# Optimization experiments

Hardware: AMD Instinct MI355X
Metric: run time of the kernel (lower is better)

Reference implementation:

```python
import jax, jax.numpy as jnp
import numpy as np

N_HEAD = 16
N_KV_HEAD = 4
HEAD_DIM = 128
RMS_EPS = 1.1920928955078125e-07  # torch float32 eps used by F.rms_norm default


def apply_rotary_emb(x, cos, sin):
    # x: [B,T,H,D]; cos/sin: [1,T,1,D/2]
    d = x.shape[-1] // 2
    x1, x2 = x[..., :d], x[..., d:]
    return jnp.concatenate([x1 * cos + x2 * sin, -x1 * sin + x2 * cos], axis=-1)


def rms_norm(x):
    return x * jax.lax.rsqrt(jnp.mean(x * x, axis=-1, keepdims=True) + RMS_EPS)


def setup_inputs() -> dict:
    key = jax.random.key(0)
    ks = jax.random.split(key, 7)
    B, T, C = 2, 2048, 2048
    return {
        "x": jax.random.normal(ks[0], (B, T, C), jnp.float32),
        "cos": jax.random.normal(ks[1], (1, T, 1, HEAD_DIM // 2), jnp.float32),
        "sin": jax.random.normal(ks[2], (1, T, 1, HEAD_DIM // 2), jnp.float32),
        "wq": jax.random.normal(ks[3], (C, N_HEAD * HEAD_DIM), jnp.float32) * 0.02,
        "wk": jax.random.normal(ks[4], (C, N_KV_HEAD * HEAD_DIM), jnp.float32) * 0.02,
        "wv": jax.random.normal(ks[5], (C, N_KV_HEAD * HEAD_DIM), jnp.float32) * 0.02,
        "wo": jax.random.normal(ks[6], (C, C), jnp.float32) * 0.02,
        "window_size": 512,
    }


def reference(x, cos, sin, wq, wk, wv, wo, window_size):
    B, T, C = x.shape
    H, KV, D = N_HEAD, N_KV_HEAD, HEAD_DIM
    rep = H // KV
    q = (x @ wq).reshape(B, T, H, D)
    k = (x @ wk).reshape(B, T, KV, D)
    v = (x @ wv).reshape(B, T, KV, D)
    q = rms_norm(apply_rotary_emb(q, cos, sin))
    k = rms_norm(apply_rotary_emb(k, cos, sin))
    # GQA: group query heads by kv head instead of materializing expanded K/V
    qg = q.reshape(B, T, KV, rep, D)
    scale = 1.0 / np.sqrt(D)
    scores = jnp.einsum('btkrd,bskd->bkrts', qg, k) * scale  # [B,KV,rep,T,S]
    row = jnp.arange(T)[:, None]
    col = jnp.arange(T)[None, :]
    mask = (col <= row) & (row - col <= window_size)  # causal & sliding window
    scores = jnp.where(mask, scores, jnp.finfo(scores.dtype).min)
    probs = jax.nn.softmax(scores, axis=-1)
    y = jnp.einsum('bkrts,bskd->btkrd', probs, v).reshape(B, T, H * D)
    return y @ wo
```

## Files before the change

kernel.cpp:

```cpp
#include <hip/hip_runtime.h>
#include <stdint.h>

typedef __attribute__((ext_vector_type(4))) float f32x4;
typedef __attribute__((ext_vector_type(8))) __bf16 bf16x8;
typedef __attribute__((ext_vector_type(4))) unsigned int u32x4;
typedef unsigned short u16;

#define B_DIM 2
#define T_DIM 2048
#define C_DIM 2048
#define H_Q   16
#define H_KV  4
#define HD    128
#define NQKV  3072
#define MTOK  4096
#define RMS_EPS 1.1920928955078125e-07f
#define Q_SCALE 0.12751749f

__device__ __forceinline__ u16 f2bf(float f) {
  union { float f; unsigned int u; } v; v.f = f;
  unsigned int r = v.u + 0x7FFFu + ((v.u >> 16) & 1u);
  return (u16)(r >> 16);
}
__device__ __forceinline__ float bf2f(u16 h) {
  union { unsigned int u; float f; } v; v.u = ((unsigned int)h) << 16;
  return v.f;
}
__device__ __forceinline__ f32x4 mfma16(bf16x8 a, bf16x8 b, f32x4 c) {
  return __builtin_amdgcn_mfma_f32_16x16x32_bf16(a, b, c, 0, 0, 0);
}
__device__ __forceinline__ void gl_lds16(const void* g, void* l) {
  __builtin_amdgcn_global_load_lds(
      (const __attribute__((address_space(1))) unsigned int*)g,
      (__attribute__((address_space(3))) unsigned int*)l, 16, 0, 0);
}

__global__ __launch_bounds__(256) void prep_kernel(const float* __restrict__ x,
                                                   const float* __restrict__ wq,
                                                   const float* __restrict__ wk,
                                                   const float* __restrict__ wv,
                                                   const float* __restrict__ wo,
                                                   u16* __restrict__ xb,
                                                   u16* __restrict__ wqkvb,
                                                   u16* __restrict__ wob) {
  __shared__ float tile[64][65];
  int bid = blockIdx.x, t = threadIdx.x;
  if (bid < 2560) {
    int nb = bid % 80, kb = bid / 80;
    const float* src; u16* dst; int srcN, nloc;
    if (nb < 32)      { src = wq; srcN = 2048; nloc = nb;      dst = wqkvb; }
    else if (nb < 40) { src = wk; srcN = 512;  nloc = nb - 32; dst = wqkvb + (size_t)2048 * 2048; }
    else if (nb < 48) { src = wv; srcN = 512;  nloc = nb - 40; dst = wqkvb + (size_t)2560 * 2048; }
    else              { src = wo; srcN = 2048; nloc = nb - 48; dst = wob; }
    int n0 = nloc * 64, k0 = kb * 64;
    #pragma unroll
    for (int idx = t; idx < 4096; idx += 256) {
      int r = idx >> 6, c = idx & 63;
      tile[r][c] = src[(size_t)(k0 + r) * srcN + n0 + c];
    }
    __syncthreads();
    #pragma unroll
    for (int idx = t; idx < 4096; idx += 256) {
      int r = idx >> 6, c = idx & 63;
      dst[(size_t)(n0 + r) * 2048 + k0 + c] = f2bf(tile[c][r]);
    }
  } else {
    int i = ((bid - 2560) * 256 + t) * 4;
    if (i >= MTOK * C_DIM) return;
    float4 v = *(const float4*)(x + i);
    u16 o0 = f2bf(v.x), o1 = f2bf(v.y), o2 = f2bf(v.z), o3 = f2bf(v.w);
    unsigned int lo = (unsigned int)o0 | ((unsigned int)o1 << 16);
    unsigned int hi = (unsigned int)o2 | ((unsigned int)o3 << 16);
    *(uint2*)(xb + i) = make_uint2(lo, hi);
  }
}

__global__ __launch_bounds__(256) void ropevt_kernel(u16* __restrict__ qkv,
                                                     const float* __restrict__ cosb,
                                                     const float* __restrict__ sinb,
                                                     u16* __restrict__ vt) {
  __shared__ __align__(16) u16 tile[64][136];
  int bid = blockIdx.x, tid = threadIdx.x;
  if (bid < 256) {
    int tt0 = (bid & 31) * 64;
    int kvh = (bid >> 5) & 3;
    int b   = bid >> 7;
    const u16* vp = qkv + ((size_t)b * T_DIM + tt0) * NQKV + C_DIM + H_KV * HD + kvh * HD;
    #pragma unroll
    for (int i = 0; i < 4; ++i) {
      int cid = tid + i * 256;
      int r = cid >> 4, c = cid & 15;
      u32x4 v = *(const u32x4*)(vp + (size_t)r * NQKV + c * 8);
      *(u32x4*)&tile[r][c * 8] = v;
    }
    __syncthreads();
    u16* op = vt + ((size_t)(b * H_KV + kvh) * HD) * T_DIM + tt0;
    #pragma unroll
    for (int i = 0; i < 4; ++i) {
      int cid = tid + i * 256;
      int d = cid >> 3, tc = cid & 7;
      u16 vals[8];
      #pragma unroll
      for (int j = 0; j < 8; ++j) vals[j] = tile[tc * 8 + j][d];
      u32x4 w;
      w.x = (unsigned int)vals[0] | ((unsigned int)vals[1] << 16);
      w.y = (unsigned int)vals[2] | ((unsigned int)vals[3] << 16);
      w.z = (unsigned int)vals[4] | ((unsigned int)vals[5] << 16);
      w.w = (unsigned int)vals[6] | ((unsigned int)vals[7] << 16);
      *(u32x4*)(op + (size_t)d * T_DIM + tc * 8) = w;
    }
  } else {
    int gw = ((bid - 256) * 256 + tid) >> 6;
    int lane = tid & 63;
    int hh = gw % (H_Q + H_KV);
    int tok = gw / (H_Q + H_KV);
    int t = tok & (T_DIM - 1);
    bool isq = (hh < H_Q);
    int base = isq ? hh * HD : (C_DIM + (hh - H_Q) * HD);
    u16* p = qkv + (size_t)tok * NQKV + base;
    float x1 = bf2f(p[lane]);
    float x2 = bf2f(p[lane + 64]);
    float c = cosb[t * 64 + lane];
    float s = sinb[t * 64 + lane];
    float o1 =  x1 * c + x2 * s;
    float o2 = -x1 * s + x2 * c;
    float ss = o1 * o1 + o2 * o2;
    #pragma unroll
    for (int off = 1; off < 64; off <<= 1) ss += __shfl_xor(ss, off);
    float r = rsqrtf(ss * (1.0f / 128.0f) + RMS_EPS);
    if (isq) r *= Q_SCALE;
    p[lane]      = f2bf(o1 * r);
    p[lane + 64] = f2bf(o2 * r);
  }
}

template<int BF16OUT>
__global__ __launch_bounds__(512) void gemm256_kernel(const u16* __restrict__ A,
                                                      const u16* __restrict__ Bt,
                                                      void* __restrict__ Cv,
                                                      int M, int N, int K) {
  __shared__ __align__(16) u16 L[2][2][2][8192];
  const int tid = threadIdx.x, lane = tid & 63, wid = tid >> 6;
  const int l15 = lane & 15, l4 = lane >> 4;
  const int nbn = N >> 8;
  const int nwg = gridDim.x;
  const int cpx = nwg >> 3;
  const int swz = (blockIdx.x & 7) * cpx + (blockIdx.x >> 3);
  const int m0 = (swz / nbn) << 8, n0 = (swz % nbn) << 8;
  const int wm = (wid >> 2) << 7;
  const int wn = (wid & 3) << 6;
  const int rbA = wm >> 4;
  const int rbB = wn >> 4;
  const int rbS = wid * 2;

  const int NT = K >> 6;
  f32x4 acc[8][4] = {};

  const u16* Ag = A  + (size_t)(m0 + rbS * 16 + l15) * K + l4 * 8;
  const u16* Bg = Bt + (size_t)(n0 + rbS * 16 + l15) * K + l4 * 8;
  const size_t rowK = (size_t)16 * K;

  auto stage_half = [&](int t, int kh, int buf) {
    int koff = t * 64 + kh * 32;
    gl_lds16(Ag + koff,        &L[buf][kh][0][(size_t)rbS * 512]);
    gl_lds16(Ag + rowK + koff, &L[buf][kh][0][(size_t)(rbS + 1) * 512]);
    gl_lds16(Bg + koff,        &L[buf][kh][1][(size_t)rbS * 512]);
    gl_lds16(Bg + rowK + koff, &L[buf][kh][1][(size_t)(rbS + 1) * 512]);
  };

  stage_half(0, 0, 0);
  stage_half(0, 1, 0);
  asm volatile("s_waitcnt vmcnt(4)" ::: "memory");
  __builtin_amdgcn_s_barrier();

  int cur = 0;
  for (int t = 0; t < NT; ++t) {
    int tn = (t < NT - 1) ? t + 1 : t;
    int nxt = cur ^ 1;
    #pragma unroll
    for (int kh = 0; kh < 2; ++kh) {
      stage_half(tn, kh, nxt);
      bf16x8 a[8], bb[4];
      #pragma unroll
      for (int mf = 0; mf < 8; ++mf)
        a[mf] = __builtin_bit_cast(bf16x8,
            *(const u32x4*)&L[cur][kh][0][(size_t)(rbA + mf) * 512 + lane * 8]);
      #pragma unroll
      for (int nf = 0; nf < 4; ++nf)
        bb[nf] = __builtin_bit_cast(bf16x8,
            *(const u32x4*)&L[cur][kh][1][(size_t)(rbB + nf) * 512 + lane * 8]);
      __builtin_amdgcn_s_setprio(1);
      #pragma unroll
      for (int mf = 0; mf < 8; ++mf)
        #pragma unroll
        for (int nf = 0; nf < 4; ++nf)
          acc[mf][nf] = mfma16(a[mf], bb[nf], acc[mf][nf]);
      __builtin_amdgcn_s_setprio(0);
      asm volatile("s_waitcnt vmcnt(4)" ::: "memory");
      __builtin_amdgcn_s_barrier();
    }
    cur = nxt;
  }
  asm volatile("s_waitcnt vmcnt(0)" ::: "memory");

  #pragma unroll
  for (int mf = 0; mf < 8; ++mf)
    #pragma unroll
    for (int nf = 0; nf < 4; ++nf)
      #pragma unroll
      for (int reg = 0; reg < 4; ++reg) {
        int row = m0 + wm + mf * 16 + l4 * 4 + reg;
        int col = n0 + wn + nf * 16 + l15;
        float v = acc[mf][nf][reg];
        if (BF16OUT) ((u16*)Cv)[(size_t)row * N + col] = f2bf(v);
        else         ((float*)Cv)[(size_t)row * N + col] = v;
      }
}

template<int BF16OUT>
__global__ __launch_bounds__(256) void gemm_bt_kernel(const u16* __restrict__ A,
                                                      const u16* __restrict__ Bt,
                                                      void* __restrict__ Cv,
                                                      int M, int N, int K) {
  __shared__ __align__(16) u16 Asm[128 * 64];
  __shared__ __align__(16) u16 Bsm[128 * 64];
  const int tid = threadIdx.x;
  const int lane = tid & 63;
  const int wid = tid >> 6;
  const int m0 = blockIdx.y * 128, n0 = blockIdx.x * 128;
  const int wm = (wid >> 1) * 64, wn = (wid & 1) * 64;
  const int l15 = lane & 15, l4 = lane >> 4;
  const int csrc = (lane & 7) ^ (lane >> 3);
  f32x4 acc[4][4] = {};

  for (int k0 = 0; k0 < K; k0 += 64) {
    __syncthreads();
    #pragma unroll
    for (int i = 0; i < 4; ++i) {
      int g = wid * 4 + i;
      int row = g * 8 + (lane >> 3);
      gl_lds16(A  + (size_t)(m0 + row) * K + k0 + csrc * 8, (char*)Asm + g * 1024);
      gl_lds16(Bt + (size_t)(n0 + row) * K + k0 + csrc * 8, (char*)Bsm + g * 1024);
    }
    __syncthreads();
    #pragma unroll
    for (int ks = 0; ks < 2; ++ks) {
      bf16x8 af[4], bfr[4];
      #pragma unroll
      for (int mf = 0; mf < 4; ++mf) {
        int r = wm + mf * 16 + l15;
        int bo = r * 128 + (((ks * 4 + l4) ^ (r & 7)) * 16);
        af[mf] = __builtin_bit_cast(bf16x8, *(const u32x4*)((const char*)Asm + bo));
      }
      #pragma unroll
      for (int nf = 0; nf < 4; ++nf) {
        int r = wn + nf * 16 + l15;
        int bo = r * 128 + (((ks * 4 + l4) ^ (r & 7)) * 16);
        bfr[nf] = __builtin_bit_cast(bf16x8, *(const u32x4*)((const char*)Bsm + bo));
      }
      #pragma unroll
      for (int mf = 0; mf < 4; ++mf)
        #pragma unroll
        for (int nf = 0; nf < 4; ++nf)
          acc[mf][nf] = mfma16(af[mf], bfr[nf], acc[mf][nf]);
    }
  }
  #pragma unroll
  for (int mf = 0; mf < 4; ++mf)
    #pragma unroll
    for (int nf = 0; nf < 4; ++nf)
      #pragma unroll
      for (int reg = 0; reg < 4; ++reg) {
        int row = m0 + wm + mf * 16 + l4 * 4 + reg;
        int col = n0 + wn + nf * 16 + l15;
        float v = acc[mf][nf][reg];
        if (BF16OUT) ((u16*)Cv)[(size_t)row * N + col] = f2bf(v);
        else         ((float*)Cv)[(size_t)row * N + col] = v;
      }
}

__global__ __launch_bounds__(256) void attn_kernel(const u16* __restrict__ qkv,
                                                   const u16* __restrict__ vt,
                                                   u16* __restrict__ yb,
                                                   const int* __restrict__ wsz_p) {
  __shared__ __align__(16) u16 Ksm[2][64 * 128];
  __shared__ __align__(16) u16 Vsm[2][128 * 64];
  __shared__ __align__(16) u16 Psm[4 * 16 * 64];

  const int W = wsz_p[0];
  const int tid = threadIdx.x, lane = tid & 63, wid = tid >> 6;
  const int l15 = lane & 15, l4 = lane >> 4;
  const int bid = blockIdx.x;
  const int h   = bid & 15;
  const int b   = (bid >> 4) & 1;
  const int qt  = 31 - (bid >> 5);
  const int kvh = h >> 2;
  const size_t tokb = (size_t)b * T_DIM;
  const u16* vtb = vt + ((size_t)(b * H_KV + kvh) * HD) * T_DIM;
  const int rbase = qt * 64 + wid * 16;

  auto stage = [&](int kt, int bufsel) {
    const u16* kp = qkv + (tokb + kt * 64) * NQKV + C_DIM + kvh * HD;
    #pragma unroll
    for (int i = 0; i < 4; ++i) {
      int g = wid * 4 + i;
      int row = g * 4 + (lane >> 4);
      int cs = (lane & 15) ^ (row & 15);
      gl_lds16(kp + (size_t)row * NQKV + cs * 8, (char*)Ksm[bufsel] + g * 1024);
    }
    const u16* vp = vtb + kt * 64;
    #pragma unroll
    for (int i = 0; i < 4; ++i) {
      int g = wid * 4 + i;
      int d = g * 8 + (lane >> 3);
      int cs = (lane & 7) ^ (d & 7);
      gl_lds16(vp + (size_t)d * T_DIM + cs * 8, (char*)Vsm[bufsel] + g * 1024);
    }
  };

  bf16x8 qf[4];
  {
    int r = rbase + l15;
    const u16* qp = qkv + (tokb + r) * NQKV + h * HD;
    #pragma unroll
    for (int ks = 0; ks < 4; ++ks)
      qf[ks] = __builtin_bit_cast(bf16x8, *(const u32x4*)(qp + ks * 32 + l4 * 8));
  }

  f32x4 yacc[8] = {};
  float mrow[4], lrow[4];
  #pragma unroll
  for (int rg = 0; rg < 4; ++rg) { mrow[rg] = -3.0e38f; lrow[rg] = 0.0f; }

  int smin = qt * 64 - W; if (smin < 0) smin = 0;
  const int t0 = smin >> 6;
  char* pbase = (char*)Psm + wid * 2048;

  stage(t0, 0);
  __syncthreads();
  int cur = 0;

  for (int kt = t0; kt <= qt; ++kt) {
    if (kt < qt) stage(kt + 1, cur ^ 1);

    const int slo = kt * 64;
    bool active = (slo <= rbase + 15) && ((rbase - (slo + 63)) <= W);
    if (active) {
      float Sc[4][4];
      #pragma unroll
      for (int nf = 0; nf < 4; ++nf) {
        f32x4 sa = {0.f, 0.f, 0.f, 0.f};
        int key = nf * 16 + l15;
        #pragma unroll
        for (int ks = 0; ks < 4; ++ks) {
          int bo = key * 256 + (((ks * 4 + l4) ^ (key & 15)) * 16);
          bf16x8 kf = __builtin_bit_cast(bf16x8, *(const u32x4*)((const char*)Ksm[cur] + bo));
          sa = mfma16(qf[ks], kf, sa);
        }
        #pragma unroll
        for (int rg = 0; rg < 4; ++rg) Sc[nf][rg] = sa[rg];
      }
      bool fullvalid = ((slo + 63) <= rbase) && ((rbase + 15 - slo) <= W);
      if (!fullvalid) {
        #pragma unroll
        for (int nf = 0; nf < 4; ++nf) {
          int s = slo + nf * 16 + l15;
          #pragma unroll
          for (int rg = 0; rg < 4; ++rg) {
            int r = rbase + l4 * 4 + rg;
            if (s > r || (r - s) > W) Sc[nf][rg] = -3.0e38f;
          }
        }
      }
      float tmax[4];
      #pragma unroll
      for (int rg = 0; rg < 4; ++rg) {
        float tm = fmaxf(fmaxf(Sc[0][rg], Sc[1][rg]), fmaxf(Sc[2][rg], Sc[3][rg]));
        #pragma unroll
        for (int off = 1; off < 16; off <<= 1) tm = fmaxf(tm, __shfl_xor(tm, off));
        tmax[rg] = tm;
      }
      bool small = tmax[0] <= mrow[0] + 8.f && tmax[1] <= mrow[1] + 8.f &&
                   tmax[2] <= mrow[2] + 8.f && tmax[3] <= mrow[3] + 8.f;
      if (!__all(small)) {
        f32x4 fv;
        #pragma unroll
        for (int rg = 0; rg < 4; ++rg) {
          float mnew = fmaxf(mrow[rg], tmax[rg]);
          float fm = exp2f(fmaxf(mrow[rg], -1.0e30f) - fmaxf(mnew, -1.0e30f));
          mrow[rg] = mnew;
          fv[rg] = fm;
          lrow[rg] *= fm;
        }
        #pragma unroll
        for (int nf2 = 0; nf2 < 8; ++nf2) yacc[nf2] *= fv;
      }
      float mc[4];
      #pragma unroll
      for (int rg = 0; rg < 4; ++rg) mc[rg] = fmaxf(mrow[rg], -1.0e30f);
      float rs[4] = {0.f, 0.f, 0.f, 0.f};
      #pragma unroll
      for (int nf = 0; nf < 4; ++nf)
        #pragma unroll
        for (int rg = 0; rg < 4; ++rg) {
          float pv = exp2f(Sc[nf][rg] - mc[rg]);
          unsigned int pbits = __builtin_bit_cast(unsigned int, pv);
          rs[rg] += __builtin_bit_cast(float, pbits & 0xFFFF0000u);
          int q   = l4 * 4 + rg;
          int key = nf * 16 + l15;
          int bo = q * 128 + (((key >> 3) ^ (q & 7)) * 16) + (key & 7) * 2;
          *(u16*)(pbase + bo) = (u16)(pbits >> 16);
        }
      #pragma unroll
      for (int rg = 0; rg < 4; ++rg) {
        #pragma unroll
        for (int off = 1; off < 16; off <<= 1) rs[rg] += __shfl_xor(rs[rg], off);
        lrow[rg] += rs[rg];
      }

      #pragma unroll
      for (int ks2 = 0; ks2 < 2; ++ks2) {
        int boA = l15 * 128 + (((ks2 * 4 + l4) ^ (l15 & 7)) * 16);
        bf16x8 pa = __builtin_bit_cast(bf16x8, *(const u32x4*)(pbase + boA));
        #pragma unroll
        for (int nf2 = 0; nf2 < 8; ++nf2) {
          int d = nf2 * 16 + l15;
          int boB = d * 128 + (((ks2 * 4 + l4) ^ (d & 7)) * 16);
          bf16x8 vf = __builtin_bit_cast(bf16x8, *(const u32x4*)((const char*)Vsm[cur] + boB));
          yacc[nf2] = mfma16(pa, vf, yacc[nf2]);
        }
      }
    }
    __syncthreads();
    cur ^= 1;
  }

  #pragma unroll
  for (int nf2 = 0; nf2 < 8; ++nf2)
    #pragma unroll
    for (int rg = 0; rg < 4; ++rg) {
      int r = rbase + l4 * 4 + rg;
      float v = yacc[nf2][rg] / lrow[rg];
      yb[(tokb + r) * (size_t)C_DIM + h * HD + nf2 * 16 + l15] = f2bf(v);
    }
}

extern "C" void kernel_launch(void* const* d_in, const int* in_sizes, int n_in,
                              void* d_out, int out_size, void* d_ws, size_t ws_size,
                              hipStream_t stream) {
  const float* x    = (const float*)d_in[0];
  const float* cosb = (const float*)d_in[1];
  const float* sinb = (const float*)d_in[2];
  const float* wq   = (const float*)d_in[3];
  const float* wk   = (const float*)d_in[4];
  const float* wv   = (const float*)d_in[5];
  const float* wo   = (const float*)d_in[6];
  const int*   wsz  = (const int*)d_in[7];

  char* ws = (char*)d_ws;
  u16* xb    = (u16*)(ws);
  u16* qkvb  = (u16*)(ws + (size_t)16777216);
  u16* wqkvb = (u16*)(ws + (size_t)41943040);
  u16* wob   = (u16*)(ws + (size_t)54525952);
  u16* ybuf  = (u16*)(ws + (size_t)62914560);
  u16* vtb   = (u16*)(ws);

  prep_kernel<<<2560 + 8192, 256, 0, stream>>>(x, wq, wk, wv, wo, xb, wqkvb, wob);
  gemm256_kernel<1><<<(MTOK / 256) * (NQKV / 256), 512, 0, stream>>>(xb, wqkvb, qkvb, MTOK, NQKV, C_DIM);
  ropevt_kernel<<<256 + (MTOK * (H_Q + H_KV)) / 4, 256, 0, stream>>>(qkvb, cosb, sinb, vtb);
  attn_kernel<<<B_DIM * H_Q * (T_DIM / 64), 256, 0, stream>>>(qkvb, vtb, ybuf, wsz);
  gemm_bt_kernel<0><<<dim3(C_DIM / 128, MTOK / 128), 256, 0, stream>>>(ybuf, wob, d_out, MTOK, C_DIM, C_DIM);
}
```

Measured before the change: 202.4 us.

## Restructure 256x256 GEMM main loop into four-phase interleaved staging and MFMA

The GEMM inner loop now splits each K-tile into four phases. Each phase issues one slice of global-to-LDS prefetch for the next tile, loads a smaller set of A/B fragments from LDS, and runs a 4x4 MFMA block. The goal is to keep fewer operand registers live and overlap LDS reads and global loads with matrix math more finely. The cost is extra barriers per tile and more delicate vmcnt/lgkmcnt accounting, which could stall or race if the counts are wrong.

```diff
diff --git a/kernel.cpp b/kernel.cpp
--- a/kernel.cpp
+++ b/kernel.cpp
@@ -147,59 +147,103 @@
   const int cpx = nwg >> 3;
   const int swz = (blockIdx.x & 7) * cpx + (blockIdx.x >> 3);
   const int m0 = (swz / nbn) << 8, n0 = (swz % nbn) << 8;
-  const int wm = (wid >> 2) << 7;
-  const int wn = (wid & 3) << 6;
-  const int rbA = wm >> 4;
-  const int rbB = wn >> 4;
-  const int rbS = wid * 2;
-
+  const int wm = (wid >> 2) << 7, wn = (wid & 3) << 6;
+  const int rbA = wm >> 4, rbB = wn >> 4;
   const int NT = K >> 6;
+
+  const u16* Ag = A  + (size_t)(m0 + l15) * K + l4 * 8;
+  const u16* Bg = Bt + (size_t)(n0 + l15) * K + l4 * 8;
+
   f32x4 acc[8][4] = {};
 
-  const u16* Ag = A  + (size_t)(m0 + rbS * 16 + l15) * K + l4 * 8;
-  const u16* Bg = Bt + (size_t)(n0 + rbS * 16 + l15) * K + l4 * 8;
-  const size_t rowK = (size_t)16 * K;
-
-  auto stage_half = [&](int t, int kh, int buf) {
-    int koff = t * 64 + kh * 32;
-    gl_lds16(Ag + koff,        &L[buf][kh][0][(size_t)rbS * 512]);
-    gl_lds16(Ag + rowK + koff, &L[buf][kh][0][(size_t)(rbS + 1) * 512]);
-    gl_lds16(Bg + koff,        &L[buf][kh][1][(size_t)rbS * 512]);
-    gl_lds16(Bg + rowK + koff, &L[buf][kh][1][(size_t)(rbS + 1) * 512]);
+  auto stage = [&](int tsrc, int buf, int type) {
+    int op = (type < 2) ? 1 : 0;
+    int rb;
+    if      (type == 0) rb = wid;
+    else if (type == 1) rb = 8 + wid;
+    else if (type == 2) rb = (wid & 3) + ((wid >> 2) << 3);
+    else                rb = 4 + (wid & 3) + ((wid >> 2) << 3);
+    const u16* src = (op ? Bg : Ag) + (size_t)rb * 16 * K + (size_t)tsrc * 64;
+    gl_lds16(src,      &L[buf][op][0][rb * 512]);
+    gl_lds16(src + 32, &L[buf][op][1][rb * 512]);
   };
 
-  stage_half(0, 0, 0);
-  stage_half(0, 1, 0);
-  asm volatile("s_waitcnt vmcnt(4)" ::: "memory");
+  stage(0, 0, 0); stage(0, 0, 1); stage(0, 0, 2); stage(0, 0, 3);
+  asm volatile("s_waitcnt vmcnt(2)" ::: "memory");
   __builtin_amdgcn_s_barrier();
 
-  int cur = 0;
   for (int t = 0; t < NT; ++t) {
-    int tn = (t < NT - 1) ? t + 1 : t;
-    int nxt = cur ^ 1;
-    #pragma unroll
-    for (int kh = 0; kh < 2; ++kh) {
-      stage_half(tn, kh, nxt);
-      bf16x8 a[8], bb[4];
-      #pragma unroll
-      for (int mf = 0; mf < 8; ++mf)
-        a[mf] = __builtin_bit_cast(bf16x8,
-            *(const u32x4*)&L[cur][kh][0][(size_t)(rbA + mf) * 512 + lane * 8]);
+    const int cur = t & 1, nxt = cur ^ 1;
+    const int ts = (t + 1 < NT) ? (t + 1) : t;
+    bf16x8 a[4], b0[4], b1[4];
+
+    stage(ts, nxt, 0);
+    #pragma unroll
+    for (int nf = 0; nf < 4; ++nf)
+      b0[nf] = __builtin_bit_cast(bf16x8, *(const u32x4*)&L[cur][1][0][(rbB + nf) * 512 + lane * 8]);
+    #pragma unroll
+    for (int i = 0; i < 4; ++i)
+      a[i] = __builtin_bit_cast(bf16x8, *(const u32x4*)&L[cur][0][0][(rbA + i) * 512 + lane * 8]);
+    __builtin_amdgcn_s_barrier();
+    asm volatile("s_waitcnt lgkmcnt(0)" ::: "memory");
+    __builtin_amdgcn_s_setprio(1);
+    #pragma unroll
+    for (int mf = 0; mf < 4; ++mf)
       #pragma unroll
       for (int nf = 0; nf < 4; ++nf)
-        bb[nf] = __builtin_bit_cast(bf16x8,
-            *(const u32x4*)&L[cur][kh][1][(size_t)(rbB + nf) * 512 + lane * 8]);
-      __builtin_amdgcn_s_setprio(1);
-      #pragma unroll
-      for (int mf = 0; mf < 8; ++mf)
-        #pragma unroll
-        for (int nf = 0; nf < 4; ++nf)
-          acc[mf][nf] = mfma16(a[mf], bb[nf], acc[mf][nf]);
-      __builtin_amdgcn_s_setprio(0);
-      asm volatile("s_waitcnt vmcnt(4)" ::: "memory");
-      __builtin_amdgcn_s_barrier();
-    }
-    cur = nxt;
+        acc[mf][nf] = mfma16(a[mf], b0[nf], acc[mf][nf]);
+    __builtin_amdgcn_s_setprio(0);
+    asm volatile("s_waitcnt vmcnt(2)" ::: "memory");
+    __builtin_amdgcn_s_barrier();
+
+    stage(ts, nxt, 1);
+    #pragma unroll
+    for (int i = 0; i < 4; ++i)
+      a[i] = __builtin_bit_cast(bf16x8, *(const u32x4*)&L[cur][0][0][(rbA + 4 + i) * 512 + lane * 8]);
+    __builtin_amdgcn_s_barrier();
+    asm volatile("s_waitcnt lgkmcnt(0)" ::: "memory");
+    __builtin_amdgcn_s_setprio(1);
+    #pragma unroll
+    for (int mf = 0; mf < 4; ++mf)
+      #pragma unroll
+      for (int nf = 0; nf < 4; ++nf)
+        acc[4 + mf][nf] = mfma16(a[mf], b0[nf], acc[4 + mf][nf]);
+    __builtin_amdgcn_s_setprio(0);
+    __builtin_amdgcn_s_barrier();
+
+    stage(ts, nxt, 2);
+    #pragma unroll
+    for (int nf = 0; nf < 4; ++nf)
+      b1[nf] = __builtin_bit_cast(bf16x8, *(const u32x4*)&L[cur][1][1][(rbB + nf) * 512 + lane * 8]);
+    #pragma unroll
+    for (int i = 0; i < 4; ++i)
+      a[i] = __builtin_bit_cast(bf16x8, *(const u32x4*)&L[cur][0][1][(rbA + i) * 512 + lane * 8]);
+    __builtin_amdgcn_s_barrier();
+    asm volatile("s_waitcnt lgkmcnt(0)" ::: "memory");
+    __builtin_amdgcn_s_setprio(1);
+    #pragma unroll
+    for (int mf = 0; mf < 4; ++mf)
+      #pragma unroll
+      for (int nf = 0; nf < 4; ++nf)
+        acc[mf][nf] = mfma16(a[mf], b1[nf], acc[mf][nf]);
+    __builtin_amdgcn_s_setprio(0);
+    __builtin_amdgcn_s_barrier();
+
+    stage(ts, nxt, 3);
+    #pragma unroll
+    for (int i = 0; i < 4; ++i)
+      a[i] = __builtin_bit_cast(bf16x8, *(const u32x4*)&L[cur][0][1][(rbA + 4 + i) * 512 + lane * 8]);
+    __builtin_amdgcn_s_barrier();
+    asm volatile("s_waitcnt lgkmcnt(0)" ::: "memory");
+    __builtin_amdgcn_s_setprio(1);
+    #pragma unroll
+    for (int mf = 0; mf < 4; ++mf)
+      #pragma unroll
+      for (int nf = 0; nf < 4; ++nf)
+        acc[4 + mf][nf] = mfma16(a[mf], b1[nf], acc[4 + mf][nf]);
+    __builtin_amdgcn_s_setprio(0);
+    asm volatile("s_waitcnt vmcnt(2)" ::: "memory");
+    __builtin_amdgcn_s_barrier();
   }
   asm volatile("s_waitcnt vmcnt(0)" ::: "memory");
 
```

New measurement: 202.5 us. About the same (+0.0%).
